# Kernel tuning notes

Hardware: AMD Instinct MI355X
Metric: run time of the kernel (lower is better)

## Reference

```python
import jax, jax.numpy as jnp
import numpy as np

B, L, F = 4096, 128, 64
NODE_MAX = 1024  # padding id is 0


def setup_inputs() -> dict:
    key = jax.random.key(0)
    k1, k2, k3, k4, k5, k6 = jax.random.split(key, 6)
    src_ids = jax.random.randint(k1, (B, L), 0, NODE_MAX, dtype=jnp.int64)
    dst_ids = jax.random.randint(k2, (B, L), 0, NODE_MAX, dtype=jnp.int64)
    W1 = jax.random.normal(k3, (1, F), dtype=jnp.float32)
    b1 = jax.random.normal(k4, (F,), dtype=jnp.float32)
    W2 = jax.random.normal(k5, (F, F), dtype=jnp.float32) / jnp.sqrt(F)
    b2 = jax.random.normal(k6, (F,), dtype=jnp.float32)
    return {"src_ids": src_ids, "dst_ids": dst_ids, "W1": W1, "b1": b1, "W2": W2, "b2": b2}


def _pair_counts(a, b):
    """For each element of a[bi, i]: (count of that id in a's row, count in b's row).

    Equality-based counting is exactly equivalent to np.unique counts + dict lookup
    (missing ids simply match nothing -> count 0).
    """
    self_cnt = (a[:, :, None] == a[:, None, :]).astype(jnp.float32).sum(-1)   # [B,L]
    cross_cnt = (a[:, :, None] == b[:, None, :]).astype(jnp.float32).sum(-1)  # [B,L]
    return self_cnt, cross_cnt


def _encode(freq, W1, b1, W2, b2):
    # freq: [B,L,2] -> unsqueeze to [B,L,2,1] -> MLP -> sum over the 2-axis -> [B,L,F]
    h = jax.nn.relu(freq[..., None] * W1[0] + b1)          # [B,L,2,F]
    out = jnp.einsum("blcf,fg->blcg", h, W2) + b2          # [B,L,2,F]
    return out.sum(axis=2)                                  # [B,L,F]


def reference(src_ids, dst_ids, W1, b1, W2, b2):
    src_self, src_cross = _pair_counts(src_ids, dst_ids)
    dst_self, dst_cross = _pair_counts(dst_ids, src_ids)
    src_mask = (src_ids != 0).astype(jnp.float32)[..., None]  # zero padded positions
    dst_mask = (dst_ids != 0).astype(jnp.float32)[..., None]
    # source rows: [freq in src, freq in dst]; dst rows: [freq in dst, freq in src]
    src_freq = jnp.stack([src_self, src_cross], axis=-1) * src_mask  # [B,L,2]
    dst_freq = jnp.stack([dst_self, dst_cross], axis=-1) * dst_mask  # [B,L,2]
    src_feat = _encode(src_freq, W1, b1, W2, b2)
    dst_feat = _encode(dst_freq, W1, b1, W2, b2)
    return src_feat, dst_feat
```

## Files before the change

### kernel.cpp

```cpp
#include <hip/hip_runtime.h>

#define LDIM 128
#define FDIM 64
#define NVALS 129
#define NODE_MAX 1024
#define TBYTES (NVALS * FDIM * 4)
#define TV4    (NVALS * FDIM / 4)

typedef float f32x4 __attribute__((ext_vector_type(4)));

__global__ __launch_bounds__(256) void build_table_kernel(
    const float* __restrict__ W1, const float* __restrict__ b1,
    const float* __restrict__ W2, const float* __restrict__ b2,
    float* __restrict__ T)
{
    const int t  = threadIdx.x;
    const int vi = t >> 6, g = t & 63;
    const int v  = blockIdx.x * 4 + vi;

    __shared__ float h[4][FDIM];
    h[vi][g] = fmaxf((float)v * W1[g] + b1[g], 0.0f);
    __syncthreads();

    if (v < NVALS) {
        float acc = b2[g];
#pragma unroll
        for (int f = 0; f < FDIM; ++f)
            acc = fmaf(h[vi][f], W2[f * FDIM + g], acc);
        T[v * FDIM + g] = acc;
    }
}

__global__ __launch_bounds__(256) void encode_rows_kernel(
    const int* __restrict__ src, const int* __restrict__ dst,
    const float* __restrict__ T,
    float* __restrict__ out_src, float* __restrict__ out_dst)
{
    const int b = blockIdx.x;
    const int t = threadIdx.x;

    __shared__ __align__(16) char tbl[TBYTES];
    __shared__ int ids[2 * LDIM];
    __shared__ int cnt[2 * LDIM];

    int* hist = (int*)tbl;

    const int myId = (t < LDIM) ? src[(size_t)b * LDIM + t]
                                : dst[(size_t)b * LDIM + (t - LDIM)];
    ((int4*)hist)[t]       = make_int4(0, 0, 0, 0);
    ((int4*)hist)[t + 256] = make_int4(0, 0, 0, 0);
    ids[t] = myId;
    __syncthreads();

    atomicAdd(&hist[((t >> 7) << 10) + myId], 1);
    __syncthreads();

    {
        const int self_base  = (t >> 7) << 10;
        const int cross_base = 1024 - self_base;
        int a = hist[self_base + myId];
        int c = hist[cross_base + myId];
        if (myId == 0) { a = 0; c = 0; }
        cnt[t] = a | (c << 8);
    }
    __syncthreads();

    {
        f32x4*       dstv = (f32x4*)tbl;
        const f32x4* srcv = (const f32x4*)T;
        for (int i = t; i < TV4; i += 256)
            dstv[i] = srcv[i];
    }
    __syncthreads();

    const f32x4* __restrict__ T4 = (const f32x4*)tbl;
    f32x4* __restrict__ o4s = (f32x4*)out_src;
    f32x4* __restrict__ o4d = (f32x4*)out_dst;
    const size_t rowBase = (size_t)b * (LDIM * FDIM / 4);

#pragma unroll
    for (int k = 0; k < 8; ++k) {
        const int c   = t + k * 256;
        const int pos = c >> 4;
        const int ch  = c & 15;

        const int qs = cnt[pos];
        o4s[rowBase + c] = T4[(qs & 255) * 16 + ch] + T4[(qs >> 8) * 16 + ch];

        const int qd = cnt[LDIM + pos];
        o4d[rowBase + c] = T4[(qd & 255) * 16 + ch] + T4[(qd >> 8) * 16 + ch];
    }
}

extern "C" void kernel_launch(void* const* d_in, const int* in_sizes, int n_in,
                              void* d_out, int out_size, void* d_ws, size_t ws_size,
                              hipStream_t stream)
{
    const int*   src = (const int*)d_in[0];
    const int*   dst = (const int*)d_in[1];
    const float* W1  = (const float*)d_in[2];
    const float* b1  = (const float*)d_in[3];
    const float* W2  = (const float*)d_in[4];
    const float* b2  = (const float*)d_in[5];

    float* out = (float*)d_out;
    float* T   = (float*)d_ws;

    const int B = in_sizes[0] / LDIM;
    const size_t half = (size_t)B * LDIM * FDIM;

    build_table_kernel<<<33, 256, 0, stream>>>(W1, b1, W2, b2, T);
    encode_rows_kernel<<<B, 256, 0, stream>>>(src, dst, T, out, out + half);
}
```

Measured before the change: 55.28 us.

## Fuse table build into encode kernel, computing only count values present per row

Drops the separate table-building kernel. Each block now works out which count values actually occur in its row, assigns them compact slots, and computes the MLP output only for those values into shared memory. This removes one launch and the per-block copy of the 129-entry table from global memory, and cuts shared memory use. In exchange every block redoes a 64x64 matvec per distinct count value, which is typically a handful of slots (each costs two block barriers), and reads W2 from global memory or cache in every block.

Result: faster. 50.57 us (-8.5%).

```diff
diff --git a/kernel.cpp b/kernel.cpp
--- a/kernel.cpp
+++ b/kernel.cpp
@@ -3,92 +3,97 @@
 #define LDIM 128
 #define FDIM 64
 #define NVALS 129
-#define NODE_MAX 1024
-#define TBYTES (NVALS * FDIM * 4)
-#define TV4    (NVALS * FDIM / 4)
+#define MAXSLOTS 64
 
 typedef float f32x4 __attribute__((ext_vector_type(4)));
 
-__global__ __launch_bounds__(256) void build_table_kernel(
+__global__ __launch_bounds__(256) void fused_encode_kernel(
+    const int* __restrict__ src, const int* __restrict__ dst,
     const float* __restrict__ W1, const float* __restrict__ b1,
     const float* __restrict__ W2, const float* __restrict__ b2,
-    float* __restrict__ T)
-{
-    const int t  = threadIdx.x;
-    const int vi = t >> 6, g = t & 63;
-    const int v  = blockIdx.x * 4 + vi;
-
-    __shared__ float h[4][FDIM];
-    h[vi][g] = fmaxf((float)v * W1[g] + b1[g], 0.0f);
-    __syncthreads();
-
-    if (v < NVALS) {
-        float acc = b2[g];
-#pragma unroll
-        for (int f = 0; f < FDIM; ++f)
-            acc = fmaf(h[vi][f], W2[f * FDIM + g], acc);
-        T[v * FDIM + g] = acc;
-    }
-}
-
-__global__ __launch_bounds__(256) void encode_rows_kernel(
-    const int* __restrict__ src, const int* __restrict__ dst,
-    const float* __restrict__ T,
     float* __restrict__ out_src, float* __restrict__ out_dst)
 {
     const int b = blockIdx.x;
     const int t = threadIdx.x;
 
-    __shared__ __align__(16) char tbl[TBYTES];
-    __shared__ int ids[2 * LDIM];
+    __shared__ __align__(16) float Tl[MAXSLOTS * FDIM];
+    __shared__ float h[4][FDIM];
+    __shared__ int slotOf[NVALS];
+    __shared__ int marked[MAXSLOTS];
     __shared__ int cnt[2 * LDIM];
+    __shared__ int nslots;
 
-    int* hist = (int*)tbl;
+    int* hist = (int*)Tl;
 
     const int myId = (t < LDIM) ? src[(size_t)b * LDIM + t]
                                 : dst[(size_t)b * LDIM + (t - LDIM)];
     ((int4*)hist)[t]       = make_int4(0, 0, 0, 0);
     ((int4*)hist)[t + 256] = make_int4(0, 0, 0, 0);
-    ids[t] = myId;
+    if (t < NVALS) slotOf[t] = -1;
+    if (t == 0) nslots = 0;
     __syncthreads();
 
     atomicAdd(&hist[((t >> 7) << 10) + myId], 1);
     __syncthreads();
 
+    int a, c;
     {
         const int self_base  = (t >> 7) << 10;
         const int cross_base = 1024 - self_base;
-        int a = hist[self_base + myId];
-        int c = hist[cross_base + myId];
+        a = hist[self_base + myId];
+        c = hist[cross_base + myId];
         if (myId == 0) { a = 0; c = 0; }
-        cnt[t] = a | (c << 8);
+        slotOf[a] = -2;
+        slotOf[c] = -2;
     }
     __syncthreads();
 
-    {
-        f32x4*       dstv = (f32x4*)tbl;
-        const f32x4* srcv = (const f32x4*)T;
-        for (int i = t; i < TV4; i += 256)
-            dstv[i] = srcv[i];
+    if (t < NVALS && slotOf[t] == -2) {
+        const int s = atomicAdd(&nslots, 1);
+        slotOf[t] = s;
+        marked[s] = t;
     }
     __syncthreads();
 
-    const f32x4* __restrict__ T4 = (const f32x4*)tbl;
+    cnt[t] = slotOf[a] | (slotOf[c] << 8);
+    const int ns = nslots;
+
+    const int vi = t >> 6, g = t & 63;
+    for (int s0 = 0; s0 < ns; s0 += 4) {
+        const int s = s0 + vi;
+        const bool act = (s < ns);
+        float v = 0.0f;
+        if (act) {
+            v = (float)marked[s];
+            h[vi][g] = fmaxf(v * W1[g] + b1[g], 0.0f);
+        }
+        __syncthreads();
+        if (act) {
+            float acc = b2[g];
+#pragma unroll
+            for (int f = 0; f < FDIM; ++f)
+                acc = fmaf(h[vi][f], W2[f * FDIM + g], acc);
+            Tl[s * FDIM + g] = acc;
+        }
+        __syncthreads();
+    }
+
+    const f32x4* __restrict__ T4 = (const f32x4*)Tl;
     f32x4* __restrict__ o4s = (f32x4*)out_src;
     f32x4* __restrict__ o4d = (f32x4*)out_dst;
     const size_t rowBase = (size_t)b * (LDIM * FDIM / 4);
 
 #pragma unroll
     for (int k = 0; k < 8; ++k) {
-        const int c   = t + k * 256;
-        const int pos = c >> 4;
-        const int ch  = c & 15;
+        const int ci  = t + k * 256;
+        const int pos = ci >> 4;
+        const int ch  = ci & 15;
 
         const int qs = cnt[pos];
-        o4s[rowBase + c] = T4[(qs & 255) * 16 + ch] + T4[(qs >> 8) * 16 + ch];
+        o4s[rowBase + ci] = T4[(qs & 255) * 16 + ch] + T4[((qs >> 8) & 255) * 16 + ch];
 
         const int qd = cnt[LDIM + pos];
-        o4d[rowBase + c] = T4[(qd & 255) * 16 + ch] + T4[(qd >> 8) * 16 + ch];
+        o4d[rowBase + ci] = T4[(qd & 255) * 16 + ch] + T4[((qd >> 8) & 255) * 16 + ch];
     }
 }
 
@@ -104,11 +109,10 @@
     const float* b2  = (const float*)d_in[5];
 
     float* out = (float*)d_out;
-    float* T   = (float*)d_ws;
 
     const int B = in_sizes[0] / LDIM;
     const size_t half = (size_t)B * LDIM * FDIM;
 
-    build_table_kernel<<<33, 256, 0, stream>>>(W1, b1, W2, b2, T);
-    encode_rows_kernel<<<B, 256, 0, stream>>>(src, dst, T, out, out + half);
+    fused_encode_kernel<<<B, 256, 0, stream>>>(src, dst, W1, b1, W2, b2,
+                                               out, out + half);
 }
```
